# Kernel tuning notes

Measured on AMD Instinct MI355X. Metric: run time of the kernel, lower is better.

## Reference

```python
import jax, jax.numpy as jnp
import numpy as np

N, E = 50000, 300000
IN, HID, OUT, HEADS = 768, 256, 128, 8
RELS = ("writes", "written_by", "cites")


def setup_inputs():
    ks = iter(jax.random.split(jax.random.key(0), 64))

    def nrm(shape, scale=1.0):
        return jax.random.normal(next(ks), shape, dtype=jnp.float32) * scale

    inp = {"x_paper": nrm((N, IN)), "x_author": nrm((N, IN))}
    for name in ("ei_writes", "ei_written_by", "ei_cites"):
        inp[name] = jax.random.randint(next(ks), (2, E), 0, N, dtype=jnp.int32)
    # layer 0: in=IN, out=HID, heads=HEADS
    s0 = 1.0 / np.sqrt(IN)
    inp["W0_paper"] = nrm((IN, HID), s0); inp["b0_paper"] = jnp.zeros((HID,), jnp.float32)
    inp["W0_author"] = nrm((IN, HID), s0); inp["b0_author"] = jnp.zeros((HID,), jnp.float32)
    D0 = HID // HEADS
    for rel in RELS:
        inp["a0s_" + rel] = nrm((HEADS, D0), 0.1)
        inp["a0d_" + rel] = nrm((HEADS, D0), 0.1)
    inp["Wk0"] = nrm((HID, HID), 1.0 / np.sqrt(HID)); inp["bk0"] = jnp.zeros((HID,), jnp.float32)
    inp["q0"] = nrm((HID,), 0.1)
    # layer 1 (last): in=HID, out=OUT, heads=1
    s1 = 1.0 / np.sqrt(HID)
    inp["W1_paper"] = nrm((HID, OUT), s1); inp["b1_paper"] = jnp.zeros((OUT,), jnp.float32)
    inp["W1_author"] = nrm((HID, OUT), s1); inp["b1_author"] = jnp.zeros((OUT,), jnp.float32)
    for rel in RELS:
        inp["a1s_" + rel] = nrm((1, OUT), 0.1)
        inp["a1d_" + rel] = nrm((1, OUT), 0.1)
    inp["Wk1"] = nrm((OUT, OUT), 1.0 / np.sqrt(OUT)); inp["bk1"] = jnp.zeros((OUT,), jnp.float32)
    inp["q1"] = nrm((OUT,), 0.1)
    return inp


def _han_layer(xs, proj, att, Wk, bk, q, edges, heads):
    # xs: {ntype: [N, in]}, proj: {ntype: (W, b)}, att: {rel: (a_src[H,D], a_dst[H,D])}
    C = q.shape[0]
    D = C // heads
    xh = {nt: (x @ proj[nt][0] + proj[nt][1]).reshape(-1, heads, D) for nt, x in xs.items()}
    outs = {nt: [] for nt in xs}
    for (st, rel, dt), ei in edges:
        a_s, a_d = att[rel]
        xsrc, xdst = xh[st], xh[dt]
        src, dst = ei[0], ei[1]
        n = xdst.shape[0]
        # GAT-style edge scores per head: [E, H]
        al = jax.nn.leaky_relu((xsrc * a_s).sum(-1)[src] + (xdst * a_d).sum(-1)[dst], 0.2)
        amax = jax.lax.stop_gradient(jax.ops.segment_max(al, dst, num_segments=n))
        ex = jnp.exp(al - amax[dst])
        alpha = ex / (jax.ops.segment_sum(ex, dst, num_segments=n)[dst] + 1e-16)
        msg = xsrc[src] * alpha[:, :, None]                      # [E, H, D]
        agg = jax.ops.segment_sum(msg, dst, num_segments=n)      # [n, H, D]
        outs[dt].append(jax.nn.relu(agg.reshape(n, C)))
    # semantic attention across metapaths (group)
    res = {}
    for nt, lst in outs.items():
        stk = jnp.stack(lst)                                     # [M, n, C]
        score = (q * jnp.tanh(stk @ Wk + bk).mean(axis=1)).sum(-1)
        w = jax.nn.softmax(score)                                # [M]
        res[nt] = jnp.einsum('m,mnc->nc', w, stk)
    return res


def reference(x_paper, x_author, W0_paper, b0_paper, W0_author, b0_author,
              a0s_writes, a0d_writes, a0s_written_by, a0d_written_by, a0s_cites, a0d_cites,
              Wk0, bk0, q0,
              W1_paper, b1_paper, W1_author, b1_author,
              a1s_writes, a1d_writes, a1s_written_by, a1d_written_by, a1s_cites, a1d_cites,
              Wk1, bk1, q1,
              ei_writes, ei_written_by, ei_cites):
    edges = [(("author", "writes", "paper"), ei_writes),
             (("paper", "written_by", "author"), ei_written_by),
             (("paper", "cites", "paper"), ei_cites)]
    h = _han_layer({"paper": x_paper, "author": x_author},
                   {"paper": (W0_paper, b0_paper), "author": (W0_author, b0_author)},
                   {"writes": (a0s_writes, a0d_writes),
                    "written_by": (a0s_written_by, a0d_written_by),
                    "cites": (a0s_cites, a0d_cites)},
                   Wk0, bk0, q0, edges, HEADS)
    h = {k: jax.nn.elu(v) for k, v in h.items()}
    h = _han_layer(h,
                   {"paper": (W1_paper, b1_paper), "author": (W1_author, b1_author)},
                   {"writes": (a1s_writes, a1d_writes),
                    "written_by": (a1s_written_by, a1d_written_by),
                    "cites": (a1s_cites, a1d_cites)},
                   Wk1, bk1, q1, edges, 1)

    def l2n(v):
        return v / jnp.maximum(jnp.linalg.norm(v, axis=1, keepdims=True), 1e-12)

    return (l2n(h["paper"]), l2n(h["author"]))
```

## Files before the change

kernel.cpp:

```cpp
#include <hip/hip_runtime.h>
#include <math.h>

#define NN 50000
#define NE 300000
#define DIN 768
#define DHID 256
#define DOUT 128
#define H0 8
#define D0 32
#define OFFST (NN + 4)

typedef __attribute__((ext_vector_type(8))) short bf16x8;
typedef __attribute__((ext_vector_type(8))) unsigned short u16x8;
typedef __attribute__((ext_vector_type(4))) float f32x4;

__device__ __forceinline__ unsigned short f2bf(float f) {
    unsigned u = __float_as_uint(f);
    unsigned r = (u + 0x7fffu + ((u >> 16) & 1u)) >> 16;
    return (unsigned short)r;
}
__device__ __forceinline__ float bf2f(unsigned short u) {
    return __uint_as_float(((unsigned)u) << 16);
}

__device__ __forceinline__ void gload16(const void* g, void* l) {
    __builtin_amdgcn_global_load_lds(
        (const __attribute__((address_space(1))) unsigned int*)g,
        (__attribute__((address_space(3))) unsigned int*)l, 16, 0, 0);
}

__global__ void transconv3_kernel(const float* __restrict__ Wa, const float* __restrict__ Wb,
                                  const float* __restrict__ Wc,
                                  unsigned short* __restrict__ Ta, unsigned short* __restrict__ Tb,
                                  unsigned short* __restrict__ Tc,
                                  int Kab, int Nab, int Kc, int Ncc)
{
    int y = blockIdx.y;
    const float* W = (y == 0) ? Wa : ((y == 1) ? Wb : Wc);
    unsigned short* T = (y == 0) ? Ta : ((y == 1) ? Tb : Tc);
    int K = (y == 2) ? Kc : Kab;
    int Nc = (y == 2) ? Ncc : Nab;
    int gid = blockIdx.x * 256 + threadIdx.x;
    if (gid >= K * Nc) return;
    int k = gid / Nc, n = gid - k * Nc;
    T[(size_t)n * K + k] = f2bf(W[gid]);
}

__global__ __launch_bounds__(256) void gemm_f32a_kernel(
    const float* __restrict__ A0, const float* __restrict__ A1,
    const unsigned short* __restrict__ Bt0, const unsigned short* __restrict__ Bt1,
    const float* __restrict__ bias0, const float* __restrict__ bias1,
    unsigned short* __restrict__ C0, unsigned short* __restrict__ C1,
    int M, int K, int Nc)
{
    __shared__ __align__(16) unsigned short As[2][128 * 32];
    __shared__ __align__(16) unsigned short Bs[2][128 * 32];
    const int z = blockIdx.z;
    const float* A = z ? A1 : A0;
    const unsigned short* Bt = z ? Bt1 : Bt0;
    const float* bias = z ? bias1 : bias0;
    unsigned short* C = z ? C1 : C0;
    const int t = threadIdx.x;
    const int lane = t & 63, w = t >> 6;
    const int wr = w >> 1, wc = w & 1;
    const int bm = blockIdx.y * 128, bn = blockIdx.x * 128;

    f32x4 acc[4][4];
    #pragma unroll
    for (int m = 0; m < 4; ++m)
        #pragma unroll
        for (int n = 0; n < 4; ++n)
            acc[m][n] = (f32x4){0.f, 0.f, 0.f, 0.f};

    const int c0 = w * 64 + lane, c1 = c0 + 256;
    const int row0 = c0 >> 2, row1 = c1 >> 2;
    const int g0 = (c0 & 3) ^ ((row0 >> 1) & 3);
    const int g1 = (c1 & 3) ^ ((row1 >> 1) & 3);
    const int ar0 = (bm + row0 < M) ? (bm + row0) : (M - 1);
    const int ar1 = (bm + row1 < M) ? (bm + row1) : (M - 1);
    const float* pAf0 = A + (size_t)ar0 * K + g0 * 8;
    const float* pAf1 = A + (size_t)ar1 * K + g1 * 8;
    const unsigned short* pB0 = Bt + (size_t)(bn + row0) * K + g0 * 8;
    const unsigned short* pB1 = Bt + (size_t)(bn + row1) * K + g1 * 8;

    const int rA = wr * 64 + (lane & 15);
    const int rB = wc * 64 + (lane & 15);
    const int gw = lane >> 4;
    const int nt = K >> 5;

    {
        float4 a0 = *(const float4*)(pAf0);
        float4 b0 = *(const float4*)(pAf0 + 4);
        float4 a1 = *(const float4*)(pAf1);
        float4 b1 = *(const float4*)(pAf1 + 4);
        gload16(pB0, &Bs[0][c0 * 8]);
        gload16(pB1, &Bs[0][c1 * 8]);
        u16x8 o0, o1;
        o0[0] = f2bf(a0.x); o0[1] = f2bf(a0.y); o0[2] = f2bf(a0.z); o0[3] = f2bf(a0.w);
        o0[4] = f2bf(b0.x); o0[5] = f2bf(b0.y); o0[6] = f2bf(b0.z); o0[7] = f2bf(b0.w);
        o1[0] = f2bf(a1.x); o1[1] = f2bf(a1.y); o1[2] = f2bf(a1.z); o1[3] = f2bf(a1.w);
        o1[4] = f2bf(b1.x); o1[5] = f2bf(b1.y); o1[6] = f2bf(b1.z); o1[7] = f2bf(b1.w);
        *(u16x8*)&As[0][c0 * 8] = o0;
        *(u16x8*)&As[0][c1 * 8] = o1;
    }
    __syncthreads();

    for (int ti = 0; ti < nt; ++ti) {
        const int cur = ti & 1;
        const int nb = cur ^ 1;
        float4 a0, b0, a1, b1;
        bool pf = (ti + 1 < nt);
        if (pf) {
            const int nk = (ti + 1) << 5;
            a0 = *(const float4*)(pAf0 + nk);
            b0 = *(const float4*)(pAf0 + nk + 4);
            a1 = *(const float4*)(pAf1 + nk);
            b1 = *(const float4*)(pAf1 + nk + 4);
            gload16(pB0 + nk, &Bs[nb][c0 * 8]);
            gload16(pB1 + nk, &Bs[nb][c1 * 8]);
        }
        bf16x8 afr[4], bfr[4];
        #pragma unroll
        for (int m = 0; m < 4; ++m) {
            int r = rA + m * 16;
            afr[m] = *(const bf16x8*)&As[cur][r * 32 + ((gw ^ ((r >> 1) & 3)) * 8)];
        }
        #pragma unroll
        for (int n = 0; n < 4; ++n) {
            int r = rB + n * 16;
            bfr[n] = *(const bf16x8*)&Bs[cur][r * 32 + ((gw ^ ((r >> 1) & 3)) * 8)];
        }
        #pragma unroll
        for (int m = 0; m < 4; ++m)
            #pragma unroll
            for (int n = 0; n < 4; ++n)
                acc[m][n] = __builtin_amdgcn_mfma_f32_16x16x32_bf16(afr[m], bfr[n], acc[m][n], 0, 0, 0);
        if (pf) {
            u16x8 o0, o1;
            o0[0] = f2bf(a0.x); o0[1] = f2bf(a0.y); o0[2] = f2bf(a0.z); o0[3] = f2bf(a0.w);
            o0[4] = f2bf(b0.x); o0[5] = f2bf(b0.y); o0[6] = f2bf(b0.z); o0[7] = f2bf(b0.w);
            o1[0] = f2bf(a1.x); o1[1] = f2bf(a1.y); o1[2] = f2bf(a1.z); o1[3] = f2bf(a1.w);
            o1[4] = f2bf(b1.x); o1[5] = f2bf(b1.y); o1[6] = f2bf(b1.z); o1[7] = f2bf(b1.w);
            *(u16x8*)&As[nb][c0 * 8] = o0;
            *(u16x8*)&As[nb][c1 * 8] = o1;
        }
        __syncthreads();
    }
    #pragma unroll
    for (int m = 0; m < 4; ++m) {
        #pragma unroll
        for (int j = 0; j < 4; ++j) {
            int row = bm + wr * 64 + m * 16 + (lane >> 4) * 4 + j;
            if (row >= M) continue;
            #pragma unroll
            for (int n = 0; n < 4; ++n) {
                int col = bn + wc * 64 + n * 16 + (lane & 15);
                C[(size_t)row * Nc + col] = f2bf(acc[m][n][j] + bias[col]);
            }
        }
    }
}

__global__ __launch_bounds__(256) void gemm_bf16_kernel(
    const unsigned short* __restrict__ A0, const unsigned short* __restrict__ A1,
    const unsigned short* __restrict__ Bt0, const unsigned short* __restrict__ Bt1,
    const float* __restrict__ bias0, const float* __restrict__ bias1,
    unsigned short* __restrict__ C0, unsigned short* __restrict__ C1,
    int M, int K, int Nc)
{
    __shared__ __align__(16) unsigned short As[2][128 * 32];
    __shared__ __align__(16) unsigned short Bs[2][128 * 32];
    const int z = blockIdx.z;
    const unsigned short* A  = z ? A1  : A0;
    const unsigned short* Bt = z ? Bt1 : Bt0;
    const float* bias = z ? bias1 : bias0;
    unsigned short* C = z ? C1 : C0;
    const int t = threadIdx.x;
    const int lane = t & 63, w = t >> 6;
    const int wr = w >> 1, wc = w & 1;
    const int bm = blockIdx.y * 128, bn = blockIdx.x * 128;

    f32x4 acc[4][4];
    #pragma unroll
    for (int m = 0; m < 4; ++m)
        #pragma unroll
        for (int n = 0; n < 4; ++n)
            acc[m][n] = (f32x4){0.f, 0.f, 0.f, 0.f};

    const int c0 = w * 64 + lane, c1 = c0 + 256;
    const int row0 = c0 >> 2, row1 = c1 >> 2;
    const int g0 = (c0 & 3) ^ ((row0 >> 1) & 3);
    const int g1 = (c1 & 3) ^ ((row1 >> 1) & 3);
    const int ar0 = (bm + row0 < M) ? (bm + row0) : (M - 1);
    const int ar1 = (bm + row1 < M) ? (bm + row1) : (M - 1);
    const unsigned short* pA0 = A + (size_t)ar0 * K + g0 * 8;
    const unsigned short* pA1 = A + (size_t)ar1 * K + g1 * 8;
    const unsigned short* pB0 = Bt + (size_t)(bn + row0) * K + g0 * 8;
    const unsigned short* pB1 = Bt + (size_t)(bn + row1) * K + g1 * 8;

    const int rA = wr * 64 + (lane & 15);
    const int rB = wc * 64 + (lane & 15);
    const int gw = lane >> 4;
    const int nt = K >> 5;

    gload16(pA0, &As[0][c0 * 8]);
    gload16(pA1, &As[0][c1 * 8]);
    gload16(pB0, &Bs[0][c0 * 8]);
    gload16(pB1, &Bs[0][c1 * 8]);
    __syncthreads();
    for (int ti = 0; ti < nt; ++ti) {
        const int cur = ti & 1;
        if (ti + 1 < nt) {
            const int nk = (ti + 1) << 5;
            const int nb = cur ^ 1;
            gload16(pA0 + nk, &As[nb][c0 * 8]);
            gload16(pA1 + nk, &As[nb][c1 * 8]);
            gload16(pB0 + nk, &Bs[nb][c0 * 8]);
            gload16(pB1 + nk, &Bs[nb][c1 * 8]);
        }
        bf16x8 afr[4], bfr[4];
        #pragma unroll
        for (int m = 0; m < 4; ++m) {
            int r = rA + m * 16;
            afr[m] = *(const bf16x8*)&As[cur][r * 32 + ((gw ^ ((r >> 1) & 3)) * 8)];
        }
        #pragma unroll
        for (int n = 0; n < 4; ++n) {
            int r = rB + n * 16;
            bfr[n] = *(const bf16x8*)&Bs[cur][r * 32 + ((gw ^ ((r >> 1) & 3)) * 8)];
        }
        #pragma unroll
        for (int m = 0; m < 4; ++m)
            #pragma unroll
            for (int n = 0; n < 4; ++n)
                acc[m][n] = __builtin_amdgcn_mfma_f32_16x16x32_bf16(afr[m], bfr[n], acc[m][n], 0, 0, 0);
        __syncthreads();
    }
    #pragma unroll
    for (int m = 0; m < 4; ++m) {
        #pragma unroll
        for (int j = 0; j < 4; ++j) {
            int row = bm + wr * 64 + m * 16 + (lane >> 4) * 4 + j;
            if (row >= M) continue;
            #pragma unroll
            for (int n = 0; n < 4; ++n) {
                int col = bn + wc * 64 + n * 16 + (lane & 15);
                C[(size_t)row * Nc + col] = f2bf(acc[m][n][j] + bias[col]);
            }
        }
    }
}

__global__ __launch_bounds__(256) void sem_bf16_kernel(
    const unsigned short* __restrict__ A, const unsigned short* __restrict__ Bt,
    const float* __restrict__ bk, float* __restrict__ partial,
    int M, int K, int Nc)
{
    __shared__ __align__(16) unsigned short As[2][128 * 32];
    __shared__ __align__(16) unsigned short Bs[2][128 * 32];
    __shared__ float red[128];
    const int t = threadIdx.x;
    const int lane = t & 63, w = t >> 6;
    const int wr = w >> 1, wc = w & 1;
    const int bm = blockIdx.y * 128, bn = blockIdx.x * 128;

    f32x4 acc[4][4];
    #pragma unroll
    for (int m = 0; m < 4; ++m)
        #pragma unroll
        for (int n = 0; n < 4; ++n)
            acc[m][n] = (f32x4){0.f, 0.f, 0.f, 0.f};

    const int c0 = w * 64 + lane, c1 = c0 + 256;
    const int row0 = c0 >> 2, row1 = c1 >> 2;
    const int g0 = (c0 & 3) ^ ((row0 >> 1) & 3);
    const int g1 = (c1 & 3) ^ ((row1 >> 1) & 3);
    const int ar0 = (bm + row0 < M) ? (bm + row0) : (M - 1);
    const int ar1 = (bm + row1 < M) ? (bm + row1) : (M - 1);
    const unsigned short* pA0 = A + (size_t)ar0 * K + g0 * 8;
    const unsigned short* pA1 = A + (size_t)ar1 * K + g1 * 8;
    const unsigned short* pB0 = Bt + (size_t)(bn + row0) * K + g0 * 8;
    const unsigned short* pB1 = Bt + (size_t)(bn + row1) * K + g1 * 8;

    const int rA = wr * 64 + (lane & 15);
    const int rB = wc * 64 + (lane & 15);
    const int gw = lane >> 4;
    const int nt = K >> 5;

    gload16(pA0, &As[0][c0 * 8]);
    gload16(pA1, &As[0][c1 * 8]);
    gload16(pB0, &Bs[0][c0 * 8]);
    gload16(pB1, &Bs[0][c1 * 8]);
    __syncthreads();
    for (int ti = 0; ti < nt; ++ti) {
        const int cur = ti & 1;
        if (ti + 1 < nt) {
            const int nk = (ti + 1) << 5;
            const int nb = cur ^ 1;
            gload16(pA0 + nk, &As[nb][c0 * 8]);
            gload16(pA1 + nk, &As[nb][c1 * 8]);
            gload16(pB0 + nk, &Bs[nb][c0 * 8]);
            gload16(pB1 + nk, &Bs[nb][c1 * 8]);
        }
        bf16x8 afr[4], bfr[4];
        #pragma unroll
        for (int m = 0; m < 4; ++m) {
            int r = rA + m * 16;
            afr[m] = *(const bf16x8*)&As[cur][r * 32 + ((gw ^ ((r >> 1) & 3)) * 8)];
        }
        #pragma unroll
        for (int n = 0; n < 4; ++n) {
            int r = rB + n * 16;
            bfr[n] = *(const bf16x8*)&Bs[cur][r * 32 + ((gw ^ ((r >> 1) & 3)) * 8)];
        }
        #pragma unroll
        for (int m = 0; m < 4; ++m)
            #pragma unroll
            for (int n = 0; n < 4; ++n)
                acc[m][n] = __builtin_amdgcn_mfma_f32_16x16x32_bf16(afr[m], bfr[n], acc[m][n], 0, 0, 0);
        __syncthreads();
    }
    if (t < 128) red[t] = 0.f;
    __syncthreads();
    #pragma unroll
    for (int n = 0; n < 4; ++n) {
        int lcol = wc * 64 + n * 16 + (lane & 15);
        float b = bk[bn + lcol];
        float s = 0.f;
        #pragma unroll
        for (int m = 0; m < 4; ++m) {
            #pragma unroll
            for (int j = 0; j < 4; ++j) {
                int row = bm + wr * 64 + m * 16 + (lane >> 4) * 4 + j;
                if (row < M) s += tanhf(acc[m][n][j] + b);
            }
        }
        atomicAdd(&red[lcol], s);
    }
    __syncthreads();
    if (t < 128) atomicAdd(&partial[bn + t], red[t]);
}

__global__ void hist3_kernel(const int* __restrict__ d0, const int* __restrict__ d1,
                             const int* __restrict__ d2, int* __restrict__ deg3)
{
    int gid = blockIdx.x * 256 + threadIdx.x;
    if (gid >= 3 * NE) return;
    int rel = gid / NE, e = gid - rel * NE;
    const int* dst = (rel == 0) ? d0 : ((rel == 1) ? d1 : d2);
    atomicAdd(&deg3[rel * NN + dst[e]], 1);
}

__global__ void block_sum3_kernel(const int* __restrict__ deg3, int* __restrict__ bsum3)
{
    __shared__ int buf[256];
    int rel = blockIdx.y;
    int i = blockIdx.x * 256 + threadIdx.x;
    buf[threadIdx.x] = (i < NN) ? deg3[rel * NN + i] : 0;
    __syncthreads();
    for (int s = 128; s > 0; s >>= 1) {
        if (threadIdx.x < s) buf[threadIdx.x] += buf[threadIdx.x + s];
        __syncthreads();
    }
    if (threadIdx.x == 0) bsum3[rel * 256 + blockIdx.x] = buf[0];
}

__global__ void scan_bsum3_kernel(const int* __restrict__ bsum3, int* __restrict__ boff3, int nb)
{
    __shared__ int buf[256];
    int rel = blockIdx.y;
    int tid = threadIdx.x;
    int v = (tid < nb) ? bsum3[rel * 256 + tid] : 0;
    buf[tid] = v;
    __syncthreads();
    for (int off = 1; off < 256; off <<= 1) {
        int t = (tid >= off) ? buf[tid - off] : 0;
        __syncthreads();
        buf[tid] += t;
        __syncthreads();
    }
    if (tid < nb) boff3[rel * 256 + tid] = buf[tid] - v;
}

__global__ void scan_final3_kernel(const int* __restrict__ deg3, const int* __restrict__ boff3,
                                   int* __restrict__ offs3)
{
    __shared__ int buf[256];
    int rel = blockIdx.y;
    int tid = threadIdx.x, b = blockIdx.x;
    int i = b * 256 + tid;
    int v = (i < NN) ? deg3[rel * NN + i] : 0;
    buf[tid] = v;
    __syncthreads();
    for (int off = 1; off < 256; off <<= 1) {
        int t = (tid >= off) ? buf[tid - off] : 0;
        __syncthreads();
        buf[tid] += t;
        __syncthreads();
    }
    int* offs = offs3 + rel * OFFST;
    if (i < NN) offs[i] = boff3[rel * 256 + b] + buf[tid] - v;
    if (i == NN - 1) offs[NN] = boff3[rel * 256 + b] + buf[tid];
}

__global__ void place3_kernel(const int* __restrict__ s0, const int* __restrict__ s1,
                              const int* __restrict__ s2,
                              const int* __restrict__ offs3, int* __restrict__ cnt3,
                              int* __restrict__ esrc3)
{
    int rel = blockIdx.y;
    int e = blockIdx.x * 256 + threadIdx.x;
    if (e >= NE) return;
    const int* srcdst = (rel == 0) ? s0 : ((rel == 1) ? s1 : s2);
    int src = srcdst[e];
    int d = srcdst[NE + e];
    int p = offs3[rel * OFFST + d] + atomicAdd(&cnt3[rel * NN + d], 1);
    esrc3[rel * NE + p] = src;
}

__global__ void scores_L0_kernel(
    const unsigned short* __restrict__ xp, const unsigned short* __restrict__ xa,
    const float* __restrict__ a_dw, const float* __restrict__ a_swb,
    const float* __restrict__ a_sc, const float* __restrict__ a_dc,
    const float* __restrict__ a_sw, const float* __restrict__ a_dwb,
    float* __restrict__ sW_dst, float* __restrict__ sWB_src,
    float* __restrict__ sC_src, float* __restrict__ sC_dst,
    float* __restrict__ sW_src, float* __restrict__ sWB_dst)
{
    int gid = blockIdx.x * 256 + threadIdx.x;
    int half = NN * H0;
    if (gid >= 2 * half) return;
    if (gid < half) {
        int node = gid >> 3, h = gid & 7;
        const unsigned short* xr = xp + (size_t)node * DHID + h * D0;
        float xv[D0];
        #pragma unroll
        for (int j = 0; j < 4; ++j) {
            u16x8 v = ((const u16x8*)xr)[j];
            #pragma unroll
            for (int k = 0; k < 8; ++k) xv[j * 8 + k] = bf2f(v[k]);
        }
        const float* p0 = a_dw  + h * D0;
        const float* p1 = a_swb + h * D0;
        const float* p2 = a_sc  + h * D0;
        const float* p3 = a_dc  + h * D0;
        float d0 = 0.f, d1 = 0.f, d2 = 0.f, d3 = 0.f;
        #pragma unroll
        for (int k = 0; k < D0; ++k) {
            float x = xv[k];
            d0 += x * p0[k]; d1 += x * p1[k]; d2 += x * p2[k]; d3 += x * p3[k];
        }
        sW_dst[gid] = d0; sWB_src[gid] = d1; sC_src[gid] = d2; sC_dst[gid] = d3;
    } else {
        int g = gid - half;
        int node = g >> 3, h = g & 7;
        const unsigned short* xr = xa + (size_t)node * DHID + h * D0;
        float xv[D0];
        #pragma unroll
        for (int j = 0; j < 4; ++j) {
            u16x8 v = ((const u16x8*)xr)[j];
            #pragma unroll
            for (int k = 0; k < 8; ++k) xv[j * 8 + k] = bf2f(v[k]);
        }
        const float* p0 = a_sw  + h * D0;
        const float* p1 = a_dwb + h * D0;
        float d0 = 0.f, d1 = 0.f;
        #pragma unroll
        for (int k = 0; k < D0; ++k) {
            float x = xv[k];
            d0 += x * p0[k]; d1 += x * p1[k];
        }
        sW_src[g] = d0; sWB_dst[g] = d1;
    }
}

__global__ void scores_L1_kernel(
    const unsigned short* __restrict__ xp, const unsigned short* __restrict__ xa,
    const float* __restrict__ a_dw, const float* __restrict__ a_swb,
    const float* __restrict__ a_sc, const float* __restrict__ a_dc,
    const float* __restrict__ a_sw, const float* __restrict__ a_dwb,
    float* __restrict__ sW_dst, float* __restrict__ sWB_src,
    float* __restrict__ sC_src, float* __restrict__ sC_dst,
    float* __restrict__ sW_src, float* __restrict__ sWB_dst)
{
    int gid = blockIdx.x * 256 + threadIdx.x;
    if (gid >= 2 * NN) return;
    if (gid < NN) {
        const unsigned short* xr = xp + (size_t)gid * DOUT;
        float d0 = 0.f, d1 = 0.f, d2 = 0.f, d3 = 0.f;
        for (int j = 0; j < DOUT / 8; ++j) {
            u16x8 v = ((const u16x8*)xr)[j];
            #pragma unroll
            for (int k = 0; k < 8; ++k) {
                float x = bf2f(v[k]);
                int c = j * 8 + k;
                d0 += x * a_dw[c]; d1 += x * a_swb[c]; d2 += x * a_sc[c]; d3 += x * a_dc[c];
            }
        }
        sW_dst[gid] = d0; sWB_src[gid] = d1; sC_src[gid] = d2; sC_dst[gid] = d3;
    } else {
        int g = gid - NN;
        const unsigned short* xr = xa + (size_t)g * DOUT;
        float d0 = 0.f, d1 = 0.f;
        for (int j = 0; j < DOUT / 8; ++j) {
            u16x8 v = ((const u16x8*)xr)[j];
            #pragma unroll
            for (int k = 0; k < 8; ++k) {
                float x = bf2f(v[k]);
                int c = j * 8 + k;
                d0 += x * a_sw[c]; d1 += x * a_dwb[c];
            }
        }
        sW_src[g] = d0; sWB_dst[g] = d1;
    }
}

__global__ void seg_alpha3_kernel(
    const int* __restrict__ offs3, const int* __restrict__ esrc3,
    const float* __restrict__ ss0, const float* __restrict__ ss1, const float* __restrict__ ss2,
    const float* __restrict__ sd0, const float* __restrict__ sd1, const float* __restrict__ sd2,
    float* __restrict__ alpha3, int H)
{
    int rel = blockIdx.y;
    const int* offs = offs3 + rel * OFFST;
    const int* esrc = esrc3 + rel * NE;
    const float* ssrc = (rel == 0) ? ss0 : ((rel == 1) ? ss1 : ss2);
    const float* sdst = (rel == 0) ? sd0 : ((rel == 1) ? sd1 : sd2);
    float* alpha = alpha3 + (size_t)rel * NE * H0;
    int gid = blockIdx.x * 256 + threadIdx.x;
    if (gid >= NN * H) return;
    int d = gid / H, h = gid - d * H;
    int beg = offs[d], end = offs[d + 1];
    float sd = sdst[gid];
    float m = -INFINITY, den = 0.f;
    for (int i = beg; i < end; ++i) {
        int s = esrc[i];
        float v = ssrc[s * H + h] + sd;
        v = (v >= 0.f) ? v : 0.2f * v;
        if (v > m) { den = den * expf(m - v) + 1.f; m = v; }
        else       den += expf(v - m);
    }
    float inv = 1.f / (den + 1e-16f);
    for (int i = beg; i < end; ++i) {
        int s = esrc[i];
        float v = ssrc[s * H + h] + sd;
        v = (v >= 0.f) ? v : 0.2f * v;
        alpha[(size_t)i * H + h] = expf(v - m) * inv;
    }
}

template<int CPL, int HH, int DSH>
__global__ __launch_bounds__(256) void gather3_kernel(
    const int* __restrict__ offs3, const int* __restrict__ esrc3,
    const float* __restrict__ alpha3,
    const unsigned short* __restrict__ x0, const unsigned short* __restrict__ x1,
    const unsigned short* __restrict__ x2,
    unsigned short* __restrict__ o0, unsigned short* __restrict__ o1,
    unsigned short* __restrict__ o2, int C)
{
    int rel = blockIdx.y;
    const int* offs = offs3 + rel * OFFST;
    const int* esrc = esrc3 + rel * NE;
    const float* alpha = alpha3 + (size_t)rel * NE * H0;
    const unsigned short* x = (rel == 0) ? x0 : ((rel == 1) ? x1 : x2);
    unsigned short* outp = (rel == 0) ? o0 : ((rel == 1) ? o1 : o2);

    int wid = threadIdx.x >> 6, lane = threadIdx.x & 63;
    int d = blockIdx.x * 4 + wid;
    int c0 = lane * CPL;
    int h = c0 >> DSH;
    int beg = offs[d], end = offs[d + 1];
    float acc0 = 0.f, acc1 = 0.f, acc2 = 0.f, acc3 = 0.f;
    int n = end - beg;
    if (n > 0) {
        int sA = esrc[beg];
        float aA = alpha[(size_t)beg * HH + h];
        int sB = sA; float aB = 0.f;
        if (n > 1) { sB = esrc[beg + 1]; aB = alpha[(size_t)(beg + 1) * HH + h]; }
        if (CPL == 4) {
            ushort4 xc = *(const ushort4*)(x + (size_t)sA * C + c0);
            for (int i = beg; i < end; ++i) {
                ushort4 xn = xc;
                if (i + 1 < end) xn = *(const ushort4*)(x + (size_t)sB * C + c0);
                int sN = sB; float aN = 0.f;
                if (i + 2 < end) { sN = esrc[i + 2]; aN = alpha[(size_t)(i + 2) * HH + h]; }
                acc0 += aA * bf2f(xc.x); acc1 += aA * bf2f(xc.y);
                acc2 += aA * bf2f(xc.z); acc3 += aA * bf2f(xc.w);
                xc = xn; aA = aB; sB = sN; aB = aN;
            }
        } else {
            ushort2 xc = *(const ushort2*)(x + (size_t)sA * C + c0);
            for (int i = beg; i < end; ++i) {
                ushort2 xn = xc;
                if (i + 1 < end) xn = *(const ushort2*)(x + (size_t)sB * C + c0);
                int sN = sB; float aN = 0.f;
                if (i + 2 < end) { sN = esrc[i + 2]; aN = alpha[(size_t)(i + 2) * HH + h]; }
                acc0 += aA * bf2f(xc.x); acc1 += aA * bf2f(xc.y);
                xc = xn; aA = aB; sB = sN; aB = aN;
            }
        }
    }
    unsigned short* op = outp + (size_t)d * C + c0;
    if (CPL == 4) {
        ushort4 st;
        st.x = f2bf(fmaxf(acc0, 0.f)); st.y = f2bf(fmaxf(acc1, 0.f));
        st.z = f2bf(fmaxf(acc2, 0.f)); st.w = f2bf(fmaxf(acc3, 0.f));
        *(ushort4*)op = st;
    } else {
        ushort2 st;
        st.x = f2bf(fmaxf(acc0, 0.f)); st.y = f2bf(fmaxf(acc1, 0.f));
        *(ushort2*)op = st;
    }
}

__global__ void sem_weights_kernel(const float* __restrict__ partial, const float* __restrict__ q,
                                   float* __restrict__ w, int C, int n)
{
    if (threadIdx.x != 0 || blockIdx.x != 0) return;
    float inv = 1.f / (float)n;
    float s0 = 0.f, s1 = 0.f;
    for (int c = 0; c < C; ++c) {
        s0 += q[c] * partial[c] * inv;
        s1 += q[c] * partial[C + c] * inv;
    }
    float m = fmaxf(s0, s1);
    float e0 = expf(s0 - m), e1 = expf(s1 - m);
    float den = e0 + e1;
    w[0] = e0 / den;
    w[1] = e1 / den;
}

__global__ void combine2_bf16_kernel(const unsigned short* __restrict__ a,
                                     const unsigned short* __restrict__ b,
                                     const float* __restrict__ w, unsigned short* __restrict__ out,
                                     int n8)
{
    int i = blockIdx.x * 256 + threadIdx.x;
    if (i >= n8) return;
    float w0 = w[0], w1 = w[1];
    u16x8 va = ((const u16x8*)a)[i];
    u16x8 vb = ((const u16x8*)b)[i];
    u16x8 o;
    #pragma unroll
    for (int j = 0; j < 8; ++j) o[j] = f2bf(w0 * bf2f(va[j]) + w1 * bf2f(vb[j]));
    ((u16x8*)out)[i] = o;
}

__global__ __launch_bounds__(128) void final_norm_kernel(
    const unsigned short* __restrict__ aggW, const unsigned short* __restrict__ aggC,
    const unsigned short* __restrict__ aggB, const float* __restrict__ w,
    float* __restrict__ out)
{
    __shared__ float red[128];
    int row = blockIdx.x;
    int c = threadIdx.x;
    float v;
    if (row < NN) {
        size_t i = (size_t)row * DOUT + c;
        v = w[0] * bf2f(aggW[i]) + w[1] * bf2f(aggC[i]);
    } else {
        size_t i = (size_t)(row - NN) * DOUT + c;
        v = bf2f(aggB[i]);
    }
    red[c] = v * v;
    __syncthreads();
    for (int s = 64; s > 0; s >>= 1) {
        if (c < s) red[c] += red[c + s];
        __syncthreads();
    }
    float norm = sqrtf(red[0]);
    out[(size_t)row * DOUT + c] = v / fmaxf(norm, 1e-12f);
}

extern "C" void kernel_launch(void* const* d_in, const int* in_sizes, int n_in,
                              void* d_out, int out_size, void* d_ws, size_t ws_size,
                              hipStream_t stream)
{
    const float* x_paper   = (const float*)d_in[0];
    const float* x_author  = (const float*)d_in[1];
    const int*   ei_writes = (const int*)d_in[2];
    const int*   ei_wb     = (const int*)d_in[3];
    const int*   ei_cites  = (const int*)d_in[4];
    const float* W0p = (const float*)d_in[5];  const float* b0p = (const float*)d_in[6];
    const float* W0a = (const float*)d_in[7];  const float* b0a = (const float*)d_in[8];
    const float* a0s_w  = (const float*)d_in[9];  const float* a0d_w  = (const float*)d_in[10];
    const float* a0s_wb = (const float*)d_in[11]; const float* a0d_wb = (const float*)d_in[12];
    const float* a0s_c  = (const float*)d_in[13]; const float* a0d_c  = (const float*)d_in[14];
    const float* Wk0 = (const float*)d_in[15]; const float* bk0 = (const float*)d_in[16];
    const float* q0  = (const float*)d_in[17];
    const float* W1p = (const float*)d_in[18]; const float* b1p = (const float*)d_in[19];
    const float* W1a = (const float*)d_in[20]; const float* b1a = (const float*)d_in[21];
    const float* a1s_w  = (const float*)d_in[22]; const float* a1d_w  = (const float*)d_in[23];
    const float* a1s_wb = (const float*)d_in[24]; const float* a1d_wb = (const float*)d_in[25];
    const float* a1s_c  = (const float*)d_in[26]; const float* a1d_c  = (const float*)d_in[27];
    const float* Wk1 = (const float*)d_in[28]; const float* bk1 = (const float*)d_in[29];
    const float* q1  = (const float*)d_in[30];

    float* out = (float*)d_out;

    const size_t NH = (size_t)NN * DHID;
    const size_t NI = (size_t)NN * DIN;
    const size_t NO = (size_t)NN * DOUT;
    const size_t NH2 = NH * 2;
    const size_t NI2 = NI * 2;
    const size_t NO2 = NO * 2;

    char* base = (char*)d_ws;
    unsigned short* xbhP = (unsigned short*)(base + 0);
    unsigned short* xbhA = (unsigned short*)(base + NH2);
    unsigned short* aggW = (unsigned short*)(base + 2 * NH2);
    unsigned short* aggC = (unsigned short*)(base + 3 * NH2);
    unsigned short* aggB = (unsigned short*)(base + 4 * NH2);
    unsigned short* hbP  = (unsigned short*)(base + 0);
    unsigned short* hbA  = aggB;
    unsigned short* x1Pb = (unsigned short*)(base + NH2);
    unsigned short* x1Ab = (unsigned short*)(base + NH2 + NO2);
    unsigned short* agg1W = (unsigned short*)(base + 2 * NH2 + NI2);
    unsigned short* agg1C = (unsigned short*)(base + 2 * NH2 + NI2 + NO2);
    unsigned short* agg1B = (unsigned short*)(base + 2 * NH2 + NI2 + 2 * NO2);

    float* sW_src  = (float*)(base + 204800000);
    float* sW_dst  = sW_src  + NN * H0;
    float* sWB_src = sW_dst  + NN * H0;
    float* sWB_dst = sWB_src + NN * H0;
    float* sC_src  = sWB_dst + NN * H0;
    float* sC_dst  = sC_src  + NN * H0;
    float* alpha3  = (float*)(base + 214400000);
    int* ip     = (int*)(base + 243200000);
    int* offs3  = ip;  ip += 3 * OFFST;
    int* esrc3  = ip;  ip += 3 * NE;
    int* deg3   = ip;  ip += 3 * NN;
    int* bsum3  = ip;  ip += 3 * 256;
    int* boff3  = ip;  ip += 3 * 256;
    unsigned short* wt0p = (unsigned short*)ip;
    unsigned short* wt0a = wt0p + (size_t)DHID * DIN;
    unsigned short* wkt  = wt0a + (size_t)DHID * DIN;
    unsigned short* wt1p = wt0p;
    unsigned short* wt1a = wt1p + (size_t)DOUT * DHID;
    float* tsum = (float*)(wkt + (size_t)DHID * DHID);
    float* wsem = tsum + 512;

    const int NB = (NN + 255) / 256;

    hipMemsetAsync(deg3, 0, 3 * NN * sizeof(int), stream);
    hist3_kernel<<<(3 * NE + 255) / 256, 256, 0, stream>>>(ei_writes + NE, ei_wb + NE, ei_cites + NE, deg3);
    block_sum3_kernel<<<dim3(NB, 3), 256, 0, stream>>>(deg3, bsum3);
    scan_bsum3_kernel<<<dim3(1, 3), 256, 0, stream>>>(bsum3, boff3, NB);
    scan_final3_kernel<<<dim3(NB, 3), 256, 0, stream>>>(deg3, boff3, offs3);
    hipMemsetAsync(deg3, 0, 3 * NN * sizeof(int), stream);
    place3_kernel<<<dim3((NE + 255) / 256, 3), 256, 0, stream>>>(ei_writes, ei_wb, ei_cites, offs3, deg3, esrc3);

    hipMemsetAsync(tsum, 0, 512 * sizeof(float), stream);
    transconv3_kernel<<<dim3((DIN * DHID + 255) / 256, 3), 256, 0, stream>>>(
        W0p, W0a, Wk0, wt0p, wt0a, wkt, DIN, DHID, DHID, DHID);

    dim3 g0(DHID / 128, (NN + 127) / 128, 2);
    gemm_f32a_kernel<<<g0, 256, 0, stream>>>(x_paper, x_author, wt0p, wt0a, b0p, b0a, xbhP, xbhA, NN, DIN, DHID);

    scores_L0_kernel<<<(2 * NN * H0 + 255) / 256, 256, 0, stream>>>(
        xbhP, xbhA, a0d_w, a0s_wb, a0s_c, a0d_c, a0s_w, a0d_wb,
        sW_dst, sWB_src, sC_src, sC_dst, sW_src, sWB_dst);
    dim3 ga0((NN * H0 + 255) / 256, 3);
    seg_alpha3_kernel<<<ga0, 256, 0, stream>>>(
        offs3, esrc3, sW_src, sWB_src, sC_src, sW_dst, sWB_dst, sC_dst, alpha3, H0);
    dim3 gg0(NN / 4, 3);
    gather3_kernel<4, H0, 5><<<gg0, 256, 0, stream>>>(
        offs3, esrc3, alpha3, xbhA, xbhP, xbhP, aggW, aggB, aggC, DHID);

    dim3 gs0(DHID / 128, (NN + 127) / 128);
    sem_bf16_kernel<<<gs0, 256, 0, stream>>>(aggW, wkt, bk0, tsum,        NN, DHID, DHID);
    sem_bf16_kernel<<<gs0, 256, 0, stream>>>(aggC, wkt, bk0, tsum + DHID, NN, DHID, DHID);
    sem_weights_kernel<<<1, 64, 0, stream>>>(tsum, q0, wsem, DHID, NN);

    combine2_bf16_kernel<<<(int)((NH / 8 + 255) / 256), 256, 0, stream>>>(aggW, aggC, wsem, hbP, (int)(NH / 8));

    transconv3_kernel<<<dim3((DHID * DOUT + 255) / 256, 3), 256, 0, stream>>>(
        W1p, W1a, Wk1, wt1p, wt1a, wkt, DHID, DOUT, DOUT, DOUT);

    dim3 g1(DOUT / 128, (NN + 127) / 128, 2);
    gemm_bf16_kernel<<<g1, 256, 0, stream>>>(hbP, hbA, wt1p, wt1a, b1p, b1a, x1Pb, x1Ab, NN, DHID, DOUT);

    hipMemsetAsync(tsum, 0, 2 * DOUT * sizeof(float), stream);

    scores_L1_kernel<<<(2 * NN + 255) / 256, 256, 0, stream>>>(
        x1Pb, x1Ab, a1d_w, a1s_wb, a1s_c, a1d_c, a1s_w, a1d_wb,
        sW_dst, sWB_src, sC_src, sC_dst, sW_src, sWB_dst);
    dim3 ga1((NN + 255) / 256, 3);
    seg_alpha3_kernel<<<ga1, 256, 0, stream>>>(
        offs3, esrc3, sW_src, sWB_src, sC_src, sW_dst, sWB_dst, sC_dst, alpha3, 1);
    dim3 gg1(NN / 4, 3);
    gather3_kernel<2, 1, 7><<<gg1, 256, 0, stream>>>(
        offs3, esrc3, alpha3, x1Ab, x1Pb, x1Pb, agg1W, agg1B, agg1C, DOUT);

    dim3 gs1(DOUT / 128, (NN + 127) / 128);
    sem_bf16_kernel<<<gs1, 256, 0, stream>>>(agg1W, wkt, bk1, tsum,        NN, DOUT, DOUT);
    sem_bf16_kernel<<<gs1, 256, 0, stream>>>(agg1C, wkt, bk1, tsum + DOUT, NN, DOUT, DOUT);
    sem_weights_kernel<<<1, 64, 0, stream>>>(tsum, q1, wsem, DOUT, NN);

    final_norm_kernel<<<2 * NN, 128, 0, stream>>>(agg1W, agg1C, agg1B, wsem, out);
}
```

Before: 753.5 us.

## Replace LDS-staged layer-0 GEMM with direct register loads and full-width column tiles

The layer-0 projection GEMM no longer stages A and B tiles through shared memory with double buffering. Each wave now loads its MFMA fragments straight from global memory and converts fp32 to bf16 in registers. Blocks grow to 512 threads and cover all 256 output columns, so each fp32 row of x is read once instead of once per column tile. This removes LDS traffic and barriers, but operands are no longer shared between waves through LDS, which raises redundant global/L2 loads and drops explicit prefetch, making the loop more sensitive to memory latency.

New measurement: 920.0 us. 22.1% more time.

```diff
diff --git a/kernel.cpp b/kernel.cpp
--- a/kernel.cpp
+++ b/kernel.cpp
@@ -46,24 +46,23 @@
     T[(size_t)n * K + k] = f2bf(W[gid]);
 }
 
-__global__ __launch_bounds__(256) void gemm_f32a_kernel(
+__global__ __launch_bounds__(512) void gemm_f32a_reg_kernel(
     const float* __restrict__ A0, const float* __restrict__ A1,
     const unsigned short* __restrict__ Bt0, const unsigned short* __restrict__ Bt1,
     const float* __restrict__ bias0, const float* __restrict__ bias1,
     unsigned short* __restrict__ C0, unsigned short* __restrict__ C1,
     int M, int K, int Nc)
 {
-    __shared__ __align__(16) unsigned short As[2][128 * 32];
-    __shared__ __align__(16) unsigned short Bs[2][128 * 32];
-    const int z = blockIdx.z;
+    const int z = blockIdx.y;
     const float* A = z ? A1 : A0;
     const unsigned short* Bt = z ? Bt1 : Bt0;
     const float* bias = z ? bias1 : bias0;
     unsigned short* C = z ? C1 : C0;
     const int t = threadIdx.x;
     const int lane = t & 63, w = t >> 6;
-    const int wr = w >> 1, wc = w & 1;
-    const int bm = blockIdx.y * 128, bn = blockIdx.x * 128;
+    const int wr = w >> 2, wc = w & 3;
+    const int bm = blockIdx.x * 128;
+    const int ko = (lane >> 4) * 8;
 
     f32x4 acc[4][4];
     #pragma unroll
@@ -72,80 +71,49 @@
         for (int n = 0; n < 4; ++n)
             acc[m][n] = (f32x4){0.f, 0.f, 0.f, 0.f};
 
-    const int c0 = w * 64 + lane, c1 = c0 + 256;
-    const int row0 = c0 >> 2, row1 = c1 >> 2;
-    const int g0 = (c0 & 3) ^ ((row0 >> 1) & 3);
-    const int g1 = (c1 & 3) ^ ((row1 >> 1) & 3);
-    const int ar0 = (bm + row0 < M) ? (bm + row0) : (M - 1);
-    const int ar1 = (bm + row1 < M) ? (bm + row1) : (M - 1);
-    const float* pAf0 = A + (size_t)ar0 * K + g0 * 8;
-    const float* pAf1 = A + (size_t)ar1 * K + g1 * 8;
-    const unsigned short* pB0 = Bt + (size_t)(bn + row0) * K + g0 * 8;
-    const unsigned short* pB1 = Bt + (size_t)(bn + row1) * K + g1 * 8;
-
-    const int rA = wr * 64 + (lane & 15);
-    const int rB = wc * 64 + (lane & 15);
-    const int gw = lane >> 4;
+    const float* pA[4];
+    const unsigned short* pB[4];
+    #pragma unroll
+    for (int m = 0; m < 4; ++m) {
+        int row = bm + wr * 64 + m * 16 + (lane & 15);
+        if (row >= M) row = M - 1;
+        pA[m] = A + (size_t)row * K + ko;
+    }
+    #pragma unroll
+    for (int n = 0; n < 4; ++n) {
+        int col = wc * 64 + n * 16 + (lane & 15);
+        pB[n] = Bt + (size_t)col * K + ko;
+    }
+
     const int nt = K >> 5;
-
-    {
-        float4 a0 = *(const float4*)(pAf0);
-        float4 b0 = *(const float4*)(pAf0 + 4);
-        float4 a1 = *(const float4*)(pAf1);
-        float4 b1 = *(const float4*)(pAf1 + 4);
-        gload16(pB0, &Bs[0][c0 * 8]);
-        gload16(pB1, &Bs[0][c1 * 8]);
-        u16x8 o0, o1;
-        o0[0] = f2bf(a0.x); o0[1] = f2bf(a0.y); o0[2] = f2bf(a0.z); o0[3] = f2bf(a0.w);
-        o0[4] = f2bf(b0.x); o0[5] = f2bf(b0.y); o0[6] = f2bf(b0.z); o0[7] = f2bf(b0.w);
-        o1[0] = f2bf(a1.x); o1[1] = f2bf(a1.y); o1[2] = f2bf(a1.z); o1[3] = f2bf(a1.w);
-        o1[4] = f2bf(b1.x); o1[5] = f2bf(b1.y); o1[6] = f2bf(b1.z); o1[7] = f2bf(b1.w);
-        *(u16x8*)&As[0][c0 * 8] = o0;
-        *(u16x8*)&As[0][c1 * 8] = o1;
-    }
-    __syncthreads();
-
+    #pragma unroll 2
     for (int ti = 0; ti < nt; ++ti) {
-        const int cur = ti & 1;
-        const int nb = cur ^ 1;
-        float4 a0, b0, a1, b1;
-        bool pf = (ti + 1 < nt);
-        if (pf) {
-            const int nk = (ti + 1) << 5;
-            a0 = *(const float4*)(pAf0 + nk);
-            b0 = *(const float4*)(pAf0 + nk + 4);
-            a1 = *(const float4*)(pAf1 + nk);
-            b1 = *(const float4*)(pAf1 + nk + 4);
-            gload16(pB0 + nk, &Bs[nb][c0 * 8]);
-            gload16(pB1 + nk, &Bs[nb][c1 * 8]);
-        }
-        bf16x8 afr[4], bfr[4];
+        const int kk = ti * 32;
+        float4 fa[4], fb[4];
         #pragma unroll
         for (int m = 0; m < 4; ++m) {
-            int r = rA + m * 16;
-            afr[m] = *(const bf16x8*)&As[cur][r * 32 + ((gw ^ ((r >> 1) & 3)) * 8)];
-        }
-        #pragma unroll
-        for (int n = 0; n < 4; ++n) {
-            int r = rB + n * 16;
-            bfr[n] = *(const bf16x8*)&Bs[cur][r * 32 + ((gw ^ ((r >> 1) & 3)) * 8)];
+            fa[m] = *(const float4*)(pA[m] + kk);
+            fb[m] = *(const float4*)(pA[m] + kk + 4);
+        }
+        bf16x8 bfr[4];
+        #pragma unroll
+        for (int n = 0; n < 4; ++n)
+            bfr[n] = *(const bf16x8*)(pB[n] + kk);
+        bf16x8 afr[4];
+        #pragma unroll
+        for (int m = 0; m < 4; ++m) {
+            afr[m][0] = (short)f2bf(fa[m].x); afr[m][1] = (short)f2bf(fa[m].y);
+            afr[m][2] = (short)f2bf(fa[m].z); afr[m][3] = (short)f2bf(fa[m].w);
+            afr[m][4] = (short)f2bf(fb[m].x); afr[m][5] = (short)f2bf(fb[m].y);
+            afr[m][6] = (short)f2bf(fb[m].z); afr[m][7] = (short)f2bf(fb[m].w);
         }
         #pragma unroll
         for (int m = 0; m < 4; ++m)
             #pragma unroll
             for (int n = 0; n < 4; ++n)
                 acc[m][n] = __builtin_amdgcn_mfma_f32_16x16x32_bf16(afr[m], bfr[n], acc[m][n], 0, 0, 0);
-        if (pf) {
-            u16x8 o0, o1;
-            o0[0] = f2bf(a0.x); o0[1] = f2bf(a0.y); o0[2] = f2bf(a0.z); o0[3] = f2bf(a0.w);
-            o0[4] = f2bf(b0.x); o0[5] = f2bf(b0.y); o0[6] = f2bf(b0.z); o0[7] = f2bf(b0.w);
-            o1[0] = f2bf(a1.x); o1[1] = f2bf(a1.y); o1[2] = f2bf(a1.z); o1[3] = f2bf(a1.w);
-            o1[4] = f2bf(b1.x); o1[5] = f2bf(b1.y); o1[6] = f2bf(b1.z); o1[7] = f2bf(b1.w);
-            *(u16x8*)&As[nb][c0 * 8] = o0;
-            *(u16x8*)&As[nb][c1 * 8] = o1;
-        }
-        __syncthreads();
-    }
+    }
+
     #pragma unroll
     for (int m = 0; m < 4; ++m) {
         #pragma unroll
@@ -154,7 +122,7 @@
             if (row >= M) continue;
             #pragma unroll
             for (int n = 0; n < 4; ++n) {
-                int col = bn + wc * 64 + n * 16 + (lane & 15);
+                int col = wc * 64 + n * 16 + (lane & 15);
                 C[(size_t)row * Nc + col] = f2bf(acc[m][n][j] + bias[col]);
             }
         }
@@ -754,8 +722,8 @@
     transconv3_kernel<<<dim3((DIN * DHID + 255) / 256, 3), 256, 0, stream>>>(
         W0p, W0a, Wk0, wt0p, wt0a, wkt, DIN, DHID, DHID, DHID);
 
-    dim3 g0(DHID / 128, (NN + 127) / 128, 2);
-    gemm_f32a_kernel<<<g0, 256, 0, stream>>>(x_paper, x_author, wt0p, wt0a, b0p, b0a, xbhP, xbhA, NN, DIN, DHID);
+    dim3 g0((NN + 127) / 128, 2);
+    gemm_f32a_reg_kernel<<<g0, 512, 0, stream>>>(x_paper, x_author, wt0p, wt0a, b0p, b0a, xbhP, xbhA, NN, DIN, DHID);
 
     scores_L0_kernel<<<(2 * NN * H0 + 255) / 256, 256, 0, stream>>>(
         xbhP, xbhA, a0d_w, a0s_wb, a0s_c, a0d_c, a0s_w, a0d_wb,
```

## Deepen layer-0 GEMM pipeline to two-stage prefetch with explicit waitcnt barriers

Applied to the files above, without the earlier changes.

The first-layer projection GEMM is specialized to compile-time K/N, and its main loop now prefetches two K-tiles ahead. A third LDS buffer is added for B, and A registers are double-buffered. __syncthreads is replaced by inline s_waitcnt vmcnt(6)/s_barrier, so the next tile's global loads can stay in flight across the barrier, and the fully unrolled loop hides more memory latency. This costs more LDS and registers, which may reduce occupancy, and the hand-tuned vmcnt count must match the number of outstanding loads to stay correct.

Measured after the change: 750.1 us. No clear change (-0.4%).

```diff
diff --git a/kernel.cpp b/kernel.cpp
--- a/kernel.cpp
+++ b/kernel.cpp
@@ -27,6 +27,13 @@
     __builtin_amdgcn_global_load_lds(
         (const __attribute__((address_space(1))) unsigned int*)g,
         (__attribute__((address_space(3))) unsigned int*)l, 16, 0, 0);
+}
+
+__device__ __forceinline__ void store_bf8(unsigned short* dst, float4 lo, float4 hi) {
+    u16x8 o;
+    o[0] = f2bf(lo.x); o[1] = f2bf(lo.y); o[2] = f2bf(lo.z); o[3] = f2bf(lo.w);
+    o[4] = f2bf(hi.x); o[5] = f2bf(hi.y); o[6] = f2bf(hi.z); o[7] = f2bf(hi.w);
+    *(u16x8*)dst = o;
 }
 
 __global__ void transconv3_kernel(const float* __restrict__ Wa, const float* __restrict__ Wb,
@@ -46,15 +53,17 @@
     T[(size_t)n * K + k] = f2bf(W[gid]);
 }
 
-__global__ __launch_bounds__(256) void gemm_f32a_kernel(
+__global__ __launch_bounds__(256) void gemm_l0_kernel(
     const float* __restrict__ A0, const float* __restrict__ A1,
     const unsigned short* __restrict__ Bt0, const unsigned short* __restrict__ Bt1,
     const float* __restrict__ bias0, const float* __restrict__ bias1,
-    unsigned short* __restrict__ C0, unsigned short* __restrict__ C1,
-    int M, int K, int Nc)
-{
+    unsigned short* __restrict__ C0, unsigned short* __restrict__ C1)
+{
+    constexpr int K  = DIN;
+    constexpr int Nc = DHID;
+    constexpr int NT = K / 32;
     __shared__ __align__(16) unsigned short As[2][128 * 32];
-    __shared__ __align__(16) unsigned short Bs[2][128 * 32];
+    __shared__ __align__(16) unsigned short Bs[3][128 * 32];
     const int z = blockIdx.z;
     const float* A = z ? A1 : A0;
     const unsigned short* Bt = z ? Bt1 : Bt0;
@@ -72,86 +81,83 @@
         for (int n = 0; n < 4; ++n)
             acc[m][n] = (f32x4){0.f, 0.f, 0.f, 0.f};
 
-    const int c0 = w * 64 + lane, c1 = c0 + 256;
+    const int c0 = t, c1 = t + 256;
     const int row0 = c0 >> 2, row1 = c1 >> 2;
     const int g0 = (c0 & 3) ^ ((row0 >> 1) & 3);
     const int g1 = (c1 & 3) ^ ((row1 >> 1) & 3);
-    const int ar0 = (bm + row0 < M) ? (bm + row0) : (M - 1);
-    const int ar1 = (bm + row1 < M) ? (bm + row1) : (M - 1);
-    const float* pAf0 = A + (size_t)ar0 * K + g0 * 8;
-    const float* pAf1 = A + (size_t)ar1 * K + g1 * 8;
+    int ar0 = bm + row0; if (ar0 >= NN) ar0 = NN - 1;
+    int ar1 = bm + row1; if (ar1 >= NN) ar1 = NN - 1;
+    const float* pA0 = A + (size_t)ar0 * K + g0 * 8;
+    const float* pA1 = A + (size_t)ar1 * K + g1 * 8;
     const unsigned short* pB0 = Bt + (size_t)(bn + row0) * K + g0 * 8;
     const unsigned short* pB1 = Bt + (size_t)(bn + row1) * K + g1 * 8;
 
     const int rA = wr * 64 + (lane & 15);
     const int rB = wc * 64 + (lane & 15);
     const int gw = lane >> 4;
-    const int nt = K >> 5;
-
+
+    float4 ra[2][4];
     {
-        float4 a0 = *(const float4*)(pAf0);
-        float4 b0 = *(const float4*)(pAf0 + 4);
-        float4 a1 = *(const float4*)(pAf1);
-        float4 b1 = *(const float4*)(pAf1 + 4);
+        float4 t00 = *(const float4*)(pA0);
+        float4 t01 = *(const float4*)(pA0 + 4);
+        float4 t10 = *(const float4*)(pA1);
+        float4 t11 = *(const float4*)(pA1 + 4);
         gload16(pB0, &Bs[0][c0 * 8]);
         gload16(pB1, &Bs[0][c1 * 8]);
-        u16x8 o0, o1;
-        o0[0] = f2bf(a0.x); o0[1] = f2bf(a0.y); o0[2] = f2bf(a0.z); o0[3] = f2bf(a0.w);
-        o0[4] = f2bf(b0.x); o0[5] = f2bf(b0.y); o0[6] = f2bf(b0.z); o0[7] = f2bf(b0.w);
-        o1[0] = f2bf(a1.x); o1[1] = f2bf(a1.y); o1[2] = f2bf(a1.z); o1[3] = f2bf(a1.w);
-        o1[4] = f2bf(b1.x); o1[5] = f2bf(b1.y); o1[6] = f2bf(b1.z); o1[7] = f2bf(b1.w);
-        *(u16x8*)&As[0][c0 * 8] = o0;
-        *(u16x8*)&As[0][c1 * 8] = o1;
-    }
-    __syncthreads();
-
-    for (int ti = 0; ti < nt; ++ti) {
-        const int cur = ti & 1;
-        const int nb = cur ^ 1;
-        float4 a0, b0, a1, b1;
-        bool pf = (ti + 1 < nt);
-        if (pf) {
-            const int nk = (ti + 1) << 5;
-            a0 = *(const float4*)(pAf0 + nk);
-            b0 = *(const float4*)(pAf0 + nk + 4);
-            a1 = *(const float4*)(pAf1 + nk);
-            b1 = *(const float4*)(pAf1 + nk + 4);
-            gload16(pB0 + nk, &Bs[nb][c0 * 8]);
-            gload16(pB1 + nk, &Bs[nb][c1 * 8]);
+        ra[1][0] = *(const float4*)(pA0 + 32);
+        ra[1][1] = *(const float4*)(pA0 + 36);
+        ra[1][2] = *(const float4*)(pA1 + 32);
+        ra[1][3] = *(const float4*)(pA1 + 36);
+        gload16(pB0 + 32, &Bs[1][c0 * 8]);
+        gload16(pB1 + 32, &Bs[1][c1 * 8]);
+        store_bf8(&As[0][c0 * 8], t00, t01);
+        store_bf8(&As[0][c1 * 8], t10, t11);
+    }
+    asm volatile("s_waitcnt vmcnt(6) lgkmcnt(0)\n\ts_barrier" ::: "memory");
+
+    #pragma unroll
+    for (int ti = 0; ti < NT; ++ti) {
+        const int rcv = ti & 1;
+        const int con = rcv ^ 1;
+        if (ti + 2 < NT) {
+            const int nk = (ti + 2) * 32;
+            ra[rcv][0] = *(const float4*)(pA0 + nk);
+            ra[rcv][1] = *(const float4*)(pA0 + nk + 4);
+            ra[rcv][2] = *(const float4*)(pA1 + nk);
+            ra[rcv][3] = *(const float4*)(pA1 + nk + 4);
+            gload16(pB0 + nk, &Bs[(ti + 2) % 3][c0 * 8]);
+            gload16(pB1 + nk, &Bs[(ti + 2) % 3][c1 * 8]);
         }
         bf16x8 afr[4], bfr[4];
         #pragma unroll
         for (int m = 0; m < 4; ++m) {
             int r = rA + m * 16;
-            afr[m] = *(const bf16x8*)&As[cur][r * 32 + ((gw ^ ((r >> 1) & 3)) * 8)];
+            afr[m] = *(const bf16x8*)&As[rcv][r * 32 + ((gw ^ ((r >> 1) & 3)) * 8)];
         }
         #pragma unroll
         for (int n = 0; n < 4; ++n) {
             int r = rB + n * 16;
-            bfr[n] = *(const bf16x8*)&Bs[cur][r * 32 + ((gw ^ ((r >> 1) & 3)) * 8)];
+            bfr[n] = *(const bf16x8*)&Bs[ti % 3][r * 32 + ((gw ^ ((r >> 1) & 3)) * 8)];
         }
         #pragma unroll
         for (int m = 0; m < 4; ++m)
             #pragma unroll
             for (int n = 0; n < 4; ++n)
                 acc[m][n] = __builtin_amdgcn_mfma_f32_16x16x32_bf16(afr[m], bfr[n], acc[m][n], 0, 0, 0);
-        if (pf) {
-            u16x8 o0, o1;
-            o0[0] = f2bf(a0.x); o0[1] = f2bf(a0.y); o0[2] = f2bf(a0.z); o0[3] = f2bf(a0.w);
-            o0[4] = f2bf(b0.x); o0[5] = f2bf(b0.y); o0[6] = f2bf(b0.z); o0[7] = f2bf(b0.w);
-            o1[0] = f2bf(a1.x); o1[1] = f2bf(a1.y); o1[2] = f2bf(a1.z); o1[3] = f2bf(a1.w);
-            o1[4] = f2bf(b1.x); o1[5] = f2bf(b1.y); o1[6] = f2bf(b1.z); o1[7] = f2bf(b1.w);
-            *(u16x8*)&As[nb][c0 * 8] = o0;
-            *(u16x8*)&As[nb][c1 * 8] = o1;
-        }
-        __syncthreads();
-    }
+        if (ti + 1 < NT) {
+            store_bf8(&As[con][c0 * 8], ra[con][0], ra[con][1]);
+            store_bf8(&As[con][c1 * 8], ra[con][2], ra[con][3]);
+            if (ti + 2 < NT) asm volatile("s_waitcnt vmcnt(6) lgkmcnt(0)\n\ts_barrier" ::: "memory");
+            else             asm volatile("s_waitcnt vmcnt(0) lgkmcnt(0)\n\ts_barrier" ::: "memory");
+        }
+    }
+
     #pragma unroll
     for (int m = 0; m < 4; ++m) {
         #pragma unroll
         for (int j = 0; j < 4; ++j) {
             int row = bm + wr * 64 + m * 16 + (lane >> 4) * 4 + j;
-            if (row >= M) continue;
+            if (row >= NN) continue;
             #pragma unroll
             for (int n = 0; n < 4; ++n) {
                 int col = bn + wc * 64 + n * 16 + (lane & 15);
@@ -755,7 +761,7 @@
         W0p, W0a, Wk0, wt0p, wt0a, wkt, DIN, DHID, DHID, DHID);
 
     dim3 g0(DHID / 128, (NN + 127) / 128, 2);
-    gemm_f32a_kernel<<<g0, 256, 0, stream>>>(x_paper, x_author, wt0p, wt0a, b0p, b0a, xbhP, xbhA, NN, DIN, DHID);
+    gemm_l0_kernel<<<g0, 256, 0, stream>>>(x_paper, x_author, wt0p, wt0a, b0p, b0a, xbhP, xbhA);
 
     scores_L0_kernel<<<(2 * NN * H0 + 255) / 256, 256, 0, stream>>>(
         xbhP, xbhA, a0d_w, a0s_wb, a0s_c, a0d_c, a0s_w, a0d_wb,
```
